# Kernel tuning notes

Hardware: AMD Instinct MI355X
Metric: run time of the kernel (lower is better)

## Reference

```python
import jax, jax.numpy as jnp
import numpy as np

R, S, D, V, K, B, L, U, I = 20000, 64, 128, 50000, 32, 2048, 20480, 100000, 100000


def setup_inputs() -> dict:
    key = jax.random.key(0)
    ks = jax.random.split(key, 16)
    # segment ids: equal-sized history per batch element (guaranteed non-empty)
    seg = (jnp.arange(L, dtype=jnp.int32) // (L // B)).astype(jnp.int32)
    return {
        "user": jax.random.randint(ks[0], (B,), 0, U, dtype=jnp.int32),
        "item": jax.random.randint(ks[1], (B,), 0, I, dtype=jnp.int32),
        "historical_review": jax.random.randint(ks[2], (R, S), 0, V, dtype=jnp.int32),
        "historical_review_positive": jax.random.normal(ks[3], (R, D), jnp.float32),
        "user_hist_idx": jax.random.randint(ks[4], (L,), 0, R, dtype=jnp.int32),
        "user_hist_seg": seg,
        "item_hist_idx": jax.random.randint(ks[5], (L,), 0, R, dtype=jnp.int32),
        "item_hist_seg": seg,
        "word_emb": jax.random.normal(ks[6], (V, D), jnp.float32) * 0.02,
        "M_w": jax.random.normal(ks[7], (D, D), jnp.float32) * (1.0 / np.sqrt(D)),
        "M_b": jnp.zeros((D,), jnp.float32),
        "W_w": jax.random.normal(ks[8], (D, K), jnp.float32) * (1.0 / np.sqrt(D)),
        "W_b": jnp.zeros((K,), jnp.float32),
        "T_w": jax.random.normal(ks[9], (K, D), jnp.float32) * (1.0 / np.sqrt(K)),
        "T_b": jnp.zeros((D,), jnp.float32),
        "user_emb": jax.random.normal(ks[10], (U, D), jnp.float32) * 0.02,
        "item_emb": jax.random.normal(ks[11], (I, D), jnp.float32) * 0.02,
        "avg_rating": jnp.full((1,), 3.5, jnp.float32),
    }


def _segment_mean(x, seg, num_segments):
    s = jax.ops.segment_sum(x, seg, num_segments=num_segments)
    c = jax.ops.segment_sum(jnp.ones(seg.shape, x.dtype), seg, num_segments=num_segments)
    return s / jnp.maximum(c, 1.0)[:, None]


def reference(user, item, historical_review, historical_review_positive,
              user_hist_idx, user_hist_seg, item_hist_idx, item_hist_seg,
              word_emb, M_w, M_b, W_w, W_b, T_w, T_b,
              user_emb, item_emb, avg_rating):
    # --- aspect extraction (ABAE-style) over R historical reviews ---
    e_w = word_emb[historical_review]                      # [R, S, D] gather
    y_s = historical_review_positive                       # [R, D] sentence embedding
    # dx = transform_M(e_w) @ y_s  -> attention logits over words
    dx = jnp.einsum('rsd,de,re->rs', e_w, M_w, y_s) + jnp.einsum('d,rd->r', M_b, y_s)[:, None]
    ax = jax.nn.softmax(dx, axis=1)                        # [R, S]
    z_s = jnp.einsum('rsd,rs->rd', e_w, ax)                # [R, D]
    p_t = jax.nn.softmax(z_s @ W_w + W_b, axis=1)          # [R, K] aspect probs
    r_s = p_t @ T_w + T_b                                  # [R, D] aspect-based review embedding
    # --- ragged gather + mean-pool over user/item histories ---
    ua = _segment_mean(r_s[user_hist_idx], user_hist_seg, B)  # [B, D]
    ia = _segment_mean(r_s[item_hist_idx], item_hist_seg, B)  # [B, D]
    uf = user_emb[user]                                    # [B, D]
    itf = item_emb[item]                                   # [B, D]
    prediction = jnp.sum(ua * ia, axis=-1) + jnp.sum(uf * itf, axis=-1) + avg_rating[0]
    return prediction  # [B]
```

## Files before the change

kernel.cpp:

```cpp
#include <hip/hip_runtime.h>


typedef __attribute__((ext_vector_type(8))) short bf16x8;
typedef __attribute__((ext_vector_type(4))) float f32x4;
typedef __attribute__((ext_vector_type(2))) float vf2;

__device__ __forceinline__ unsigned int f2bf_rne(float x) {
  unsigned int u = __float_as_uint(x);
  return (u + 0x7fffu + ((u >> 16) & 1u)) >> 16;
}

__global__ __launch_bounds__(256) void kA0_pack(
    const float* __restrict__ Mw, const float* __restrict__ Ww,
    uint4* __restrict__ Wpk) {
  int c = blockIdx.x * 256 + threadIdx.x;
  if (c >= 2560) return;
  int cl = c & 63, g = c >> 6;
  int jt = g >> 2, ks = g & 3;
  int n = jt * 16 + (cl & 15);
  int k0 = ks * 32 + (cl >> 4) * 8;
  float v[8];
#pragma unroll
  for (int j = 0; j < 8; ++j) {
    int e = k0 + j;
    v[j] = (n < 128) ? Mw[(size_t)e * 128 + n] : Ww[(size_t)e * 32 + (n - 128)];
  }
  uint4 pk;
  pk.x = f2bf_rne(v[0]) | (f2bf_rne(v[1]) << 16);
  pk.y = f2bf_rne(v[2]) | (f2bf_rne(v[3]) << 16);
  pk.z = f2bf_rne(v[4]) | (f2bf_rne(v[5]) << 16);
  pk.w = f2bf_rne(v[6]) | (f2bf_rne(v[7]) << 16);
  Wpk[c] = pk;
}

__global__ __launch_bounds__(256, 2) void kA_mfma(
    const float* __restrict__ We, const uint4* __restrict__ Wpk,
    unsigned char* __restrict__ Z, unsigned char* __restrict__ WW8, int V) {
  __shared__ uint4 Bs[2560];
  int t = threadIdx.x;
  int L = t & 63, wid = t >> 6;

#pragma unroll
  for (int q = 0; q < 10; ++q) Bs[t + q * 256] = Wpk[t + q * 256];

  int r0 = blockIdx.x * 64;
  if (r0 > V - 64) r0 = V - 64;
  int rowA = r0 + wid * 16 + (L & 15);
  const float4* Arow = (const float4*)(We + (size_t)rowA * 128);

  float4 a[8];
#pragma unroll
  for (int ks = 0; ks < 4; ++ks) {
    int koff4 = ks * 8 + (L >> 4) * 2;
    a[ks * 2] = Arow[koff4];
    a[ks * 2 + 1] = Arow[koff4 + 1];
  }
  union { uint4 u; bf16x8 v; } A[4];
#pragma unroll
  for (int ks = 0; ks < 4; ++ks) {
    A[ks].u.x = f2bf_rne(a[ks * 2].x) | (f2bf_rne(a[ks * 2].y) << 16);
    A[ks].u.y = f2bf_rne(a[ks * 2].z) | (f2bf_rne(a[ks * 2].w) << 16);
    A[ks].u.z = f2bf_rne(a[ks * 2 + 1].x) | (f2bf_rne(a[ks * 2 + 1].y) << 16);
    A[ks].u.w = f2bf_rne(a[ks * 2 + 1].z) | (f2bf_rne(a[ks * 2 + 1].w) << 16);
  }
  __syncthreads();

  f32x4 acc[10];
#pragma unroll
  for (int jt = 0; jt < 10; ++jt) acc[jt] = (f32x4){0.f, 0.f, 0.f, 0.f};
#pragma unroll
  for (int ks = 0; ks < 4; ++ks) {
#pragma unroll
    for (int jt = 0; jt < 10; ++jt) {
      union { uint4 u; bf16x8 v; } Bf;
      Bf.u = Bs[(jt * 4 + ks) * 64 + L];
      acc[jt] = __builtin_amdgcn_mfma_f32_16x16x32_bf16(A[ks].v, Bf.v, acc[jt], 0, 0, 0);
    }
  }

#pragma unroll
  for (int jt = 0; jt < 10; ++jt) {
#pragma unroll
    for (int i = 0; i < 4; ++i) {
      float v0 = acc[jt][i] * 64.f;
      float v1 = __shfl_xor(v0, 1);
      float v2 = __shfl_xor(v0, 2);
      float v3 = __shfl_xor(v0, 3);
      if (!(L & 3)) {
        int col = jt * 16 + (L & 15);
        int orow = r0 + wid * 16 + (L >> 4) * 4 + i;
        int w8 = __builtin_amdgcn_cvt_pk_fp8_f32(v0, v1, 0, false);
        w8 = __builtin_amdgcn_cvt_pk_fp8_f32(v2, v3, w8, true);
        if (col < 128)
          *(int*)(Z + (size_t)orow * 128 + col) = w8;
        else
          *(int*)(WW8 + (size_t)orow * 32 + (col - 128)) = w8;
      }
    }
  }
}

__device__ __forceinline__ float dot_fp8_16(uint4 q, const float4* y) {
  float s = 0.f;
#pragma unroll
  for (int i = 0; i < 4; ++i) {
    unsigned int u = (&q.x)[i];
    vf2 a = __builtin_amdgcn_cvt_pk_f32_fp8(u, false);
    vf2 b = __builtin_amdgcn_cvt_pk_f32_fp8(u, true);
    float4 yv = y[i];
    s += a.x * yv.x + a.y * yv.y + b.x * yv.z + b.y * yv.w;
  }
  return s;
}

__global__ __launch_bounds__(256, 2) void k3_review(
    const int* __restrict__ hr, const float* __restrict__ Y,
    const unsigned char* __restrict__ Z, const unsigned char* __restrict__ WW8,
    const float* __restrict__ Wb, float* __restrict__ pOut, int R) {
  int t = threadIdx.x;
  int wv = t >> 6, lane = t & 63;
  int g = lane & 15, sub = lane >> 4;
  int rbase = (blockIdx.x * 4 + wv) * 2;
  int r0 = rbase < R ? rbase : R - 1;
  int r1 = rbase + 1 < R ? rbase + 1 : R - 1;

  int word0 = hr[(size_t)r0 * 64 + lane];
  int word1 = hr[(size_t)r1 * 64 + lane];

  uint4 q0[2][4], q1[2][4];
  uint2 w8[2][4];
#pragma unroll
  for (int p = 0; p < 4; ++p) {
    int wa = __shfl(word0, p * 16 + g);
    int wb = __shfl(word1, p * 16 + g);
    const unsigned char* ba = Z + (size_t)wa * 128;
    const unsigned char* bb = Z + (size_t)wb * 128;
    q0[0][p] = *(const uint4*)(ba + sub * 16);
    q1[0][p] = *(const uint4*)(ba + 64 + sub * 16);
    w8[0][p] = *(const uint2*)(WW8 + (size_t)wa * 32 + sub * 8);
    q0[1][p] = *(const uint4*)(bb + sub * 16);
    q1[1][p] = *(const uint4*)(bb + 64 + sub * 16);
    w8[1][p] = *(const uint2*)(WW8 + (size_t)wb * 32 + sub * 8);
  }
  float4 ya[2][4], yb[2][4];
#pragma unroll
  for (int i = 0; i < 4; ++i) {
    const float4* Y0 = (const float4*)(Y + (size_t)r0 * 128);
    const float4* Y1 = (const float4*)(Y + (size_t)r1 * 128);
    ya[0][i] = Y0[sub * 4 + i];
    yb[0][i] = Y0[16 + sub * 4 + i];
    ya[1][i] = Y1[sub * 4 + i];
    yb[1][i] = Y1[16 + sub * 4 + i];
  }
  const float4* Wb4 = (const float4*)Wb;
  float4 wba = Wb4[sub * 2], wbb = Wb4[sub * 2 + 1];

#pragma unroll
  for (int v = 0; v < 2; ++v) {
    int r = v ? r1 : r0;

    float dxp[4];
#pragma unroll
    for (int p = 0; p < 4; ++p) {
      float acc = dot_fp8_16(q0[v][p], ya[v]) + dot_fp8_16(q1[v][p], yb[v]);
      acc += __shfl_xor(acc, 16);
      acc += __shfl_xor(acc, 32);
      dxp[p] = acc * 0.015625f;
    }
    float dx = dxp[0];
    dx = (sub == 1) ? dxp[1] : dx;
    dx = (sub == 2) ? dxp[2] : dx;
    dx = (sub == 3) ? dxp[3] : dx;

    float m = dx;
#pragma unroll
    for (int off = 32; off; off >>= 1) m = fmaxf(m, __shfl_xor(m, off));
    float ex = __expf(dx - m);
    float sum = ex;
#pragma unroll
    for (int off = 32; off; off >>= 1) sum += __shfl_xor(sum, off);
    float ax = ex / sum;

    float lacc[8];
#pragma unroll
    for (int j = 0; j < 8; ++j) lacc[j] = 0.f;
#pragma unroll
    for (int p = 0; p < 4; ++p) {
      float axp = __shfl(ax, p * 16 + g);
      vf2 a0 = __builtin_amdgcn_cvt_pk_f32_fp8(w8[v][p].x, false);
      vf2 a1 = __builtin_amdgcn_cvt_pk_f32_fp8(w8[v][p].x, true);
      vf2 a2 = __builtin_amdgcn_cvt_pk_f32_fp8(w8[v][p].y, false);
      vf2 a3 = __builtin_amdgcn_cvt_pk_f32_fp8(w8[v][p].y, true);
      lacc[0] += axp * a0.x; lacc[1] += axp * a0.y;
      lacc[2] += axp * a1.x; lacc[3] += axp * a1.y;
      lacc[4] += axp * a2.x; lacc[5] += axp * a2.y;
      lacc[6] += axp * a3.x; lacc[7] += axp * a3.y;
    }
#pragma unroll
    for (int off = 8; off; off >>= 1) {
#pragma unroll
      for (int j = 0; j < 8; ++j) lacc[j] += __shfl_xor(lacc[j], off);
    }
    lacc[0] = lacc[0] * 0.015625f + wba.x; lacc[1] = lacc[1] * 0.015625f + wba.y;
    lacc[2] = lacc[2] * 0.015625f + wba.z; lacc[3] = lacc[3] * 0.015625f + wba.w;
    lacc[4] = lacc[4] * 0.015625f + wbb.x; lacc[5] = lacc[5] * 0.015625f + wbb.y;
    lacc[6] = lacc[6] * 0.015625f + wbb.z; lacc[7] = lacc[7] * 0.015625f + wbb.w;

    float mk = lacc[0];
#pragma unroll
    for (int j = 1; j < 8; ++j) mk = fmaxf(mk, lacc[j]);
    mk = fmaxf(mk, __shfl_xor(mk, 16));
    mk = fmaxf(mk, __shfl_xor(mk, 32));
    float ek[8], sk = 0.f;
#pragma unroll
    for (int j = 0; j < 8; ++j) { ek[j] = __expf(lacc[j] - mk); sk += ek[j]; }
    sk += __shfl_xor(sk, 16);
    sk += __shfl_xor(sk, 32);
    float inv = 1.0f / sk;

    if (g == 0) {
      float4 o0, o1;
      o0.x = ek[0] * inv; o0.y = ek[1] * inv; o0.z = ek[2] * inv; o0.w = ek[3] * inv;
      o1.x = ek[4] * inv; o1.y = ek[5] * inv; o1.z = ek[6] * inv; o1.w = ek[7] * inv;
      float* dst = pOut + (size_t)r * 32 + sub * 8;
      *(float4*)dst = o0;
      *(float4*)(dst + 4) = o1;
    }
  }
}

__global__ __launch_bounds__(256) void k4_final(
    const float* __restrict__ p, const int* __restrict__ uidx,
    const int* __restrict__ iidx, const int* __restrict__ user,
    const int* __restrict__ item, const float* __restrict__ uemb,
    const float* __restrict__ iemb, const float* __restrict__ Tw,
    const float* __restrict__ Tb, const float* __restrict__ avg,
    float* __restrict__ out, int B, int per) {
  int t = threadIdx.x;
  int w = t >> 6, lane = t & 63;
  int b = blockIdx.x * 4 + w;
  if (b >= B) return;

  int k = lane & 31;
  const int* idx = (lane < 32) ? uidx : iidx;
  float pbar = 0.f;
  int base = b * per;
  for (int j = 0; j < per; ++j) {
    int id = idx[base + j];
    pbar += p[(size_t)id * 32 + k];
  }
  pbar *= 1.0f / (float)per;

  const float2* T2 = (const float2*)Tw;
  float2 tb2 = ((const float2*)Tb)[lane];
  float2 ua = tb2, ia = tb2;
#pragma unroll 8
  for (int kk = 0; kk < 32; ++kk) {
    float pu = __shfl(pbar, kk);
    float pi = __shfl(pbar, 32 + kk);
    float2 tv = T2[kk * 64 + lane];
    ua.x += pu * tv.x; ua.y += pu * tv.y;
    ia.x += pi * tv.x; ia.y += pi * tv.y;
  }
  float part = ua.x * ia.x + ua.y * ia.y;
  float2 uf = ((const float2*)uemb)[(size_t)user[b] * 64 + lane];
  float2 itf = ((const float2*)iemb)[(size_t)item[b] * 64 + lane];
  part += uf.x * itf.x + uf.y * itf.y;
#pragma unroll
  for (int off = 32; off; off >>= 1) part += __shfl_xor(part, off);
  if (lane == 0) out[b] = part + avg[0];
}

extern "C" void kernel_launch(void* const* d_in, const int* in_sizes, int n_in,
                              void* d_out, int out_size, void* d_ws, size_t ws_size,
                              hipStream_t stream) {
  const int*   user = (const int*)d_in[0];
  const int*   item = (const int*)d_in[1];
  const int*   hr   = (const int*)d_in[2];
  const float* Y    = (const float*)d_in[3];
  const int*   uhi  = (const int*)d_in[4];
  const int*   ihi  = (const int*)d_in[6];
  const float* We   = (const float*)d_in[8];
  const float* Mw   = (const float*)d_in[9];
  const float* Ww   = (const float*)d_in[11];
  const float* Wb   = (const float*)d_in[12];
  const float* Tw   = (const float*)d_in[13];
  const float* Tb   = (const float*)d_in[14];
  const float* Ue   = (const float*)d_in[15];
  const float* Ie   = (const float*)d_in[16];
  const float* avg  = (const float*)d_in[17];

  int B = in_sizes[0];
  int R = in_sizes[3] / 128;
  int V = in_sizes[8] / 128;
  int L = in_sizes[4];
  int per = L / B;

  unsigned char* ws = (unsigned char*)d_ws;
  uint4* Wpk = (uint4*)ws;
  unsigned char* Z   = ws + 40960;
  unsigned char* WW8 = Z + (size_t)V * 128;
  float* pbuf = (float*)(WW8 + (size_t)V * 32);
  float* out = (float*)d_out;

  kA0_pack<<<10, 256, 0, stream>>>(Mw, Ww, Wpk);
  kA_mfma<<<(V + 63) / 64, 256, 0, stream>>>(We, Wpk, Z, WW8, V);
  k3_review<<<(R + 7) / 8, 256, 0, stream>>>(hr, Y, Z, WW8, Wb, pbuf, R);
  k4_final<<<(B + 3) / 4, 256, 0, stream>>>(pbuf, uhi, ihi, user, item, Ue, Ie,
                                            Tw, Tb, avg, out, B, per);
}
```

Baseline: 223.1 us.

## Write MFMA outputs in native lane layout and permute Y to match

The MFMA epilogue now writes fp8 results straight from each lane's accumulator columns in a permuted layout, dropping the cross-lane shuffles. The review kernel reads Z and y_s in that same permuted order, using a new kernel that permutes Y. The dot product switches to packed float2 multiply-adds, and the aspect/T_w indexing is remapped to the new column order. This adds an extra launch and an extra read and write of Y (about 10 MB each) in exchange for a cheaper epilogue and packed math.

```diff
diff --git a/kernel.cpp b/kernel.cpp
--- a/kernel.cpp
+++ b/kernel.cpp
@@ -33,6 +33,15 @@
   Wpk[c] = pk;
 }
 
+__global__ __launch_bounds__(256) void kY_perm(
+    const float* __restrict__ Y, float* __restrict__ Yp, int n) {
+  int i = blockIdx.x * 256 + threadIdx.x;
+  if (i >= n) return;
+  int r = i >> 7, pos = i & 127;
+  int d = ((pos & 7) << 4) + (pos >> 3);
+  Yp[i] = Y[(size_t)(r << 7) + d];
+}
+
 __global__ __launch_bounds__(256, 2) void kA_mfma(
     const float* __restrict__ We, const uint4* __restrict__ Wpk,
     unsigned char* __restrict__ Z, unsigned char* __restrict__ WW8, int V) {
@@ -78,43 +87,33 @@
     }
   }
 
-#pragma unroll
-  for (int jt = 0; jt < 10; ++jt) {
-#pragma unroll
-    for (int i = 0; i < 4; ++i) {
-      float v0 = acc[jt][i] * 64.f;
-      float v1 = __shfl_xor(v0, 1);
-      float v2 = __shfl_xor(v0, 2);
-      float v3 = __shfl_xor(v0, 3);
-      if (!(L & 3)) {
-        int col = jt * 16 + (L & 15);
-        int orow = r0 + wid * 16 + (L >> 4) * 4 + i;
-        int w8 = __builtin_amdgcn_cvt_pk_fp8_f32(v0, v1, 0, false);
-        w8 = __builtin_amdgcn_cvt_pk_fp8_f32(v2, v3, w8, true);
-        if (col < 128)
-          *(int*)(Z + (size_t)orow * 128 + col) = w8;
-        else
-          *(int*)(WW8 + (size_t)orow * 32 + (col - 128)) = w8;
-      }
-    }
-  }
-}
-
-__device__ __forceinline__ float dot_fp8_16(uint4 q, const float4* y) {
-  float s = 0.f;
+  int c = L & 15, q = L >> 4;
 #pragma unroll
   for (int i = 0; i < 4; ++i) {
-    unsigned int u = (&q.x)[i];
-    vf2 a = __builtin_amdgcn_cvt_pk_f32_fp8(u, false);
-    vf2 b = __builtin_amdgcn_cvt_pk_f32_fp8(u, true);
-    float4 yv = y[i];
-    s += a.x * yv.x + a.y * yv.y + b.x * yv.z + b.y * yv.w;
-  }
-  return s;
+    int orow = r0 + wid * 16 + q * 4 + i;
+    int dwA = __builtin_amdgcn_cvt_pk_fp8_f32(acc[0][i] * 64.f, acc[1][i] * 64.f, 0, false);
+    dwA = __builtin_amdgcn_cvt_pk_fp8_f32(acc[2][i] * 64.f, acc[3][i] * 64.f, dwA, true);
+    int dwB = __builtin_amdgcn_cvt_pk_fp8_f32(acc[4][i] * 64.f, acc[5][i] * 64.f, 0, false);
+    dwB = __builtin_amdgcn_cvt_pk_fp8_f32(acc[6][i] * 64.f, acc[7][i] * 64.f, dwB, true);
+    uint2 st; st.x = (unsigned int)dwA; st.y = (unsigned int)dwB;
+    *(uint2*)(Z + (size_t)orow * 128 + c * 8) = st;
+    int dwC = __builtin_amdgcn_cvt_pk_fp8_f32(acc[8][i] * 64.f, acc[9][i] * 64.f, 0, false);
+    *(unsigned short*)(WW8 + (size_t)orow * 32 + c * 2) = (unsigned short)dwC;
+  }
+}
+
+__device__ __forceinline__ vf2 dot_fp8_16_pk(uint4 q, const vf2* y2, vf2 acc) {
+#pragma unroll
+  for (int w = 0; w < 4; ++w) {
+    unsigned int u = (&q.x)[w];
+    acc += __builtin_amdgcn_cvt_pk_f32_fp8(u, false) * y2[2 * w];
+    acc += __builtin_amdgcn_cvt_pk_f32_fp8(u, true) * y2[2 * w + 1];
+  }
+  return acc;
 }
 
 __global__ __launch_bounds__(256, 2) void k3_review(
-    const int* __restrict__ hr, const float* __restrict__ Y,
+    const int* __restrict__ hr, const float* __restrict__ Yp,
     const unsigned char* __restrict__ Z, const unsigned char* __restrict__ WW8,
     const float* __restrict__ Wb, float* __restrict__ pOut, int R) {
   int t = threadIdx.x;
@@ -133,36 +132,37 @@
   for (int p = 0; p < 4; ++p) {
     int wa = __shfl(word0, p * 16 + g);
     int wb = __shfl(word1, p * 16 + g);
-    const unsigned char* ba = Z + (size_t)wa * 128;
-    const unsigned char* bb = Z + (size_t)wb * 128;
-    q0[0][p] = *(const uint4*)(ba + sub * 16);
-    q1[0][p] = *(const uint4*)(ba + 64 + sub * 16);
+    const unsigned char* ba = Z + (size_t)wa * 128 + sub * 32;
+    const unsigned char* bb = Z + (size_t)wb * 128 + sub * 32;
+    q0[0][p] = *(const uint4*)(ba);
+    q1[0][p] = *(const uint4*)(ba + 16);
     w8[0][p] = *(const uint2*)(WW8 + (size_t)wa * 32 + sub * 8);
-    q0[1][p] = *(const uint4*)(bb + sub * 16);
-    q1[1][p] = *(const uint4*)(bb + 64 + sub * 16);
+    q0[1][p] = *(const uint4*)(bb);
+    q1[1][p] = *(const uint4*)(bb + 16);
     w8[1][p] = *(const uint2*)(WW8 + (size_t)wb * 32 + sub * 8);
   }
-  float4 ya[2][4], yb[2][4];
-#pragma unroll
-  for (int i = 0; i < 4; ++i) {
-    const float4* Y0 = (const float4*)(Y + (size_t)r0 * 128);
-    const float4* Y1 = (const float4*)(Y + (size_t)r1 * 128);
-    ya[0][i] = Y0[sub * 4 + i];
-    yb[0][i] = Y0[16 + sub * 4 + i];
-    ya[1][i] = Y1[sub * 4 + i];
-    yb[1][i] = Y1[16 + sub * 4 + i];
+  float4 yv[2][8];
+#pragma unroll
+  for (int i = 0; i < 8; ++i) {
+    yv[0][i] = ((const float4*)(Yp + (size_t)r0 * 128))[sub * 8 + i];
+    yv[1][i] = ((const float4*)(Yp + (size_t)r1 * 128))[sub * 8 + i];
   }
   const float4* Wb4 = (const float4*)Wb;
-  float4 wba = Wb4[sub * 2], wbb = Wb4[sub * 2 + 1];
+  float4 wbe = Wb4[sub];
+  float4 wbo = Wb4[4 + sub];
 
 #pragma unroll
   for (int v = 0; v < 2; ++v) {
     int r = v ? r1 : r0;
+    const vf2* y2 = (const vf2*)yv[v];
 
     float dxp[4];
 #pragma unroll
     for (int p = 0; p < 4; ++p) {
-      float acc = dot_fp8_16(q0[v][p], ya[v]) + dot_fp8_16(q1[v][p], yb[v]);
+      vf2 a2 = {0.f, 0.f};
+      a2 = dot_fp8_16_pk(q0[v][p], y2, a2);
+      a2 = dot_fp8_16_pk(q1[v][p], y2 + 8, a2);
+      float acc = a2.x + a2.y;
       acc += __shfl_xor(acc, 16);
       acc += __shfl_xor(acc, 32);
       dxp[p] = acc * 0.015625f;
@@ -201,10 +201,10 @@
 #pragma unroll
       for (int j = 0; j < 8; ++j) lacc[j] += __shfl_xor(lacc[j], off);
     }
-    lacc[0] = lacc[0] * 0.015625f + wba.x; lacc[1] = lacc[1] * 0.015625f + wba.y;
-    lacc[2] = lacc[2] * 0.015625f + wba.z; lacc[3] = lacc[3] * 0.015625f + wba.w;
-    lacc[4] = lacc[4] * 0.015625f + wbb.x; lacc[5] = lacc[5] * 0.015625f + wbb.y;
-    lacc[6] = lacc[6] * 0.015625f + wbb.z; lacc[7] = lacc[7] * 0.015625f + wbb.w;
+    lacc[0] = lacc[0] * 0.015625f + wbe.x; lacc[1] = lacc[1] * 0.015625f + wbo.x;
+    lacc[2] = lacc[2] * 0.015625f + wbe.y; lacc[3] = lacc[3] * 0.015625f + wbo.y;
+    lacc[4] = lacc[4] * 0.015625f + wbe.z; lacc[5] = lacc[5] * 0.015625f + wbo.z;
+    lacc[6] = lacc[6] * 0.015625f + wbe.w; lacc[7] = lacc[7] * 0.015625f + wbo.w;
 
     float mk = lacc[0];
 #pragma unroll
@@ -241,13 +241,13 @@
   int b = blockIdx.x * 4 + w;
   if (b >= B) return;
 
-  int k = lane & 31;
-  const int* idx = (lane < 32) ? uidx : iidx;
+  int idx = lane & 31;
+  const int* sidx = (lane < 32) ? uidx : iidx;
   float pbar = 0.f;
   int base = b * per;
   for (int j = 0; j < per; ++j) {
-    int id = idx[base + j];
-    pbar += p[(size_t)id * 32 + k];
+    int id = sidx[base + j];
+    pbar += p[(size_t)id * 32 + idx];
   }
   pbar *= 1.0f / (float)per;
 
@@ -256,9 +256,10 @@
   float2 ua = tb2, ia = tb2;
 #pragma unroll 8
   for (int kk = 0; kk < 32; ++kk) {
+    int ka = ((kk & 1) << 4) + ((kk >> 3) << 2) + ((kk & 7) >> 1);
     float pu = __shfl(pbar, kk);
     float pi = __shfl(pbar, 32 + kk);
-    float2 tv = T2[kk * 64 + lane];
+    float2 tv = T2[ka * 64 + lane];
     ua.x += pu * tv.x; ua.y += pu * tv.y;
     ia.x += pi * tv.x; ia.y += pi * tv.y;
   }
@@ -300,12 +301,14 @@
   uint4* Wpk = (uint4*)ws;
   unsigned char* Z   = ws + 40960;
   unsigned char* WW8 = Z + (size_t)V * 128;
-  float* pbuf = (float*)(WW8 + (size_t)V * 32);
+  float* Yp   = (float*)(WW8 + (size_t)V * 32);
+  float* pbuf = Yp + (size_t)R * 128;
   float* out = (float*)d_out;
 
   kA0_pack<<<10, 256, 0, stream>>>(Mw, Ww, Wpk);
+  kY_perm<<<(R * 128 + 255) / 256, 256, 0, stream>>>(Y, Yp, R * 128);
   kA_mfma<<<(V + 63) / 64, 256, 0, stream>>>(We, Wpk, Z, WW8, V);
-  k3_review<<<(R + 7) / 8, 256, 0, stream>>>(hr, Y, Z, WW8, Wb, pbuf, R);
+  k3_review<<<(R + 7) / 8, 256, 0, stream>>>(hr, Yp, Z, WW8, Wb, pbuf, R);
   k4_final<<<(B + 3) / 4, 256, 0, stream>>>(pbuf, uhi, ihi, user, item, Ue, Ie,
                                             Tw, Tb, avg, out, B, per);
 }
```

Measured after the change: 222.1 us. Within noise of the previous version (-0.4%).
